# Optimization experiments

Measured on AMD Instinct MI355X. Metric: run time of the kernel, lower is better.

The kernel has to match this reference:

```python
import jax, jax.numpy as jnp
import numpy as np

H = W = 1024          # image_shape (square)
ZP, PH, PW = 16, 32, 32   # psf z-stack shape
THRESH = 2.0          # detection_threshold
K = 1024              # spots_per_frame
ROISIZE = PW          # default roisize = psf.shape[-1]
BG_R = PW * 2         # default bg_filter_size
MAXF = PW             # default max_filter_size


def setup_inputs() -> dict:
    key = jax.random.key(0)
    k1, k2 = jax.random.split(key)
    image = jax.random.uniform(k1, (H, W), jnp.float32) * 100.0
    psf = jax.random.uniform(k2, (ZP, PH, PW), jnp.float32)
    psf = psf / jnp.sum(psf, axis=(1, 2), keepdims=True)  # normalized PSF stack
    return {"image": image, "psf": psf}


def _precompute_filters(psf):
    pad = (H - PH) // 2  # square image/psf -> same pad both dims
    psf_padded = jnp.pad(psf, ((0, 0), (pad, pad), (pad, pad)))
    psf_padded = jnp.fft.fftshift(psf_padded, axes=(1, 2))
    psf_fd = jnp.flip(jnp.fft.fft2(psf_padded), axis=(1, 2))
    rr = (jnp.arange(H) - H // 2)[:, None] ** 2 + (jnp.arange(W) - W // 2)[None, :] ** 2
    bg = (rr < BG_R ** 2).astype(jnp.float32) / (np.pi * BG_R ** 2)
    bg_fd = jnp.fft.fft2(jnp.fft.fftshift(bg))
    return psf_fd, bg_fd


def reference(image, psf):
    psf_fd, bg_fd = _precompute_filters(psf)
    image_fd = jnp.fft.fft2(image)
    conv_psf = jnp.fft.ifft2(image_fd[None] * psf_fd).real       # [Z,H,W]
    conv_bg = jnp.fft.ifft2(image_fd * bg_fd).real               # [H,W]
    ratio = conv_psf / (conv_bg[None] + 1.0)                     # matched-filter SNR
    result = ratio.max(axis=0)                                   # [H,W]
    zmap = jnp.argmax(ratio, axis=0)                             # best z plane

    # MaxPool2d(MAXF, stride=1, padding=MAXF//2-1): torch pads with -inf,
    # output is [H-1,W-1]; torch code then zero-pads one row/col at top-left.
    p = MAXF // 2 - 1
    mx = jax.lax.reduce_window(result, -jnp.inf, jax.lax.max,
                               (MAXF, MAXF), (1, 1), ((p, p), (p, p)))
    mx = jnp.pad(mx, ((1, 0), (1, 0)))                           # back to [H,W]

    mask = jnp.where((mx == result) & (result > THRESH), result, 0.0)
    values, indices = jax.lax.top_k(mask.ravel(), K)
    x = indices % W
    y = indices // H  # torch divides by input_shape[0]; square so == W
    roy = y - ROISIZE // 2
    rox = x - ROISIZE // 2
    valid = ((values > THRESH)
             & (roy >= 0) & (roy < H - ROISIZE)
             & (rox >= 0) & (rox < W - ROISIZE))

    # fixed-shape version of boolean select: clamp for safe gather, mask invalids
    roy_c = jnp.clip(roy, 0, H - ROISIZE)
    rox_c = jnp.clip(rox, 0, W - ROISIZE)
    r = jnp.arange(ROISIZE)
    Y = roy_c[:, None, None] + r[None, :, None]                  # [K,R,1]
    X = rox_c[:, None, None] + r[None, None, :]                  # [K,1,R]
    rois = image[Y, X] * valid[:, None, None].astype(image.dtype)  # [K,R,R]

    roipos = jnp.stack((roy_c, rox_c), -1) * valid[:, None]
    intensity = values * valid
    return roipos, intensity, rois, valid
```

## Files before the change

### kernel.cpp

```cpp
#include <hip/hip_runtime.h>
#include <stdint.h>

typedef float v4f __attribute__((ext_vector_type(4)));
typedef int   v8i __attribute__((ext_vector_type(8)));

#define PEX_STRIDE 1156
#define CSTRIDE 858
#define WS_IMG8   0
#define WS_BFRAG  1048576
#define WS_PEX    1064960
#define WS_RESULT 9994240
#define WS_CAND   14188544

__device__ inline unsigned char f32_to_e4m3(float v) {
    if (!(v > 0.0f)) return 0;
    if (v >= 448.0f) return 0x7e;
    if (v < 0.015625f) {
        int m = (int)(v * 512.0f + 0.5f);
        if (m > 7) return 0x08;
        return (unsigned char)m;
    }
    unsigned int u = __float_as_uint(v) + 0x00080000u;
    int e = (int)((u >> 23) & 0xff) - 127;
    int m3 = (int)(u >> 20) & 7;
    int e8 = e + 7;
    if (e8 >= 16) return 0x7e;
    return (unsigned char)((e8 << 3) | m3);
}

__global__ void k_pex(const float* __restrict__ img, float* __restrict__ pex,
                      uint32_t* __restrict__ img8, const float* __restrict__ psf,
                      unsigned char* __restrict__ bf, unsigned int* cnt,
                      float4* __restrict__ out, int n4) {
    __shared__ float wtot[4];
    int blk = blockIdx.x, t = threadIdx.x;
    if (blk >= 1024) {
        if (blk < 2080) {
            int i = (blk - 1024) * 256 + t;
            if (i < n4) { float4 z; z.x = z.y = z.z = z.w = 0.f; out[i] = z; }
        } else {
            int u = (blk - 2080) * 256 + t;
            if (u == 0) cnt[0] = 0u;
            int kb4 = u >> 11; int l = (u >> 5) & 63; int b = u & 31;
            int z = l & 15; int a = kb4 * 4 + (l >> 4);
            float p = psf[z * 1024 + a * 32 + b];
            float c = cosf((float)(a + b - 32) * (6.283185307179586f / 1024.0f));
            bf[u] = f32_to_e4m3(p * c * 1024.0f);
        }
        return;
    }
    int r = blk;
    const float* row = img + r * 1024;
    float s[5];
    float acc = 0.f;
    int base = t * 5;
    #pragma unroll
    for (int j = 0; j < 5; j++) {
        int c = base + j;
        float v = (c < 1152) ? row[(c - 64) & 1023] : 0.f;
        acc += v; s[j] = acc;
    }
    float sc = acc;
    int lane = t & 63, w = t >> 6;
    #pragma unroll
    for (int off = 1; off < 64; off <<= 1) {
        float v = __shfl_up(sc, off, 64);
        if (lane >= off) sc += v;
    }
    if (lane == 63) wtot[w] = sc;
    __syncthreads();
    float wbase = 0.f;
    #pragma unroll
    for (int i = 0; i < 3; i++) if (i < w) wbase += wtot[i];
    float excl = wbase + (sc - acc);
    float* prow = pex + r * PEX_STRIDE;
    if (t == 0) prow[0] = 0.f;
    #pragma unroll
    for (int j = 0; j < 5; j++) {
        int c = base + j;
        if (c < 1152) prow[c + 1] = excl + s[j];
    }
    float4 v4 = *(const float4*)(row + 4 * t);
    img8[r * 256 + t] = (uint32_t)f32_to_e4m3(v4.x)
                      | ((uint32_t)f32_to_e4m3(v4.y) << 8)
                      | ((uint32_t)f32_to_e4m3(v4.z) << 16)
                      | ((uint32_t)f32_to_e4m3(v4.w) << 24);
}

__device__ inline v8i ldsB(const unsigned long long* p) {
    unsigned long long q0 = p[0], q1 = p[1], q2 = p[2], q3 = p[3];
    v8i v;
    v[0] = (int)(unsigned int)q0;  v[1] = (int)(unsigned int)(q0 >> 32);
    v[2] = (int)(unsigned int)q1;  v[3] = (int)(unsigned int)(q1 >> 32);
    v[4] = (int)(unsigned int)q2;  v[5] = (int)(unsigned int)(q2 >> 32);
    v[6] = (int)(unsigned int)q3;  v[7] = (int)(unsigned int)(q3 >> 32);
    return v;
}

__global__ __launch_bounds__(512, 4) void k_conv(
    const unsigned long long* __restrict__ img64,
    const unsigned char* __restrict__ bfrag,
    const float* __restrict__ pex, float* __restrict__ result) {
    __shared__ unsigned long long sm[8 * CSTRIDE];
    __shared__ float rbp[8][5][8];
    __shared__ float rbv[8][5];
    int tid = threadIdx.x;
    int wave = tid >> 6, lane = tid & 63;
    int b = blockIdx.x;
    int tr = b >> 5, tc = b & 31;
    int r0 = tr * 64, c0 = tc * 32;

    if (lane < 40) {
        int si = lane / 5, kc = lane - si * 5;
        int baserow = r0 + si * 8 + 3;
        int n = c0 + 8 * kc;
        int j0 = wave * 16;
        float acc = 0.f;
        #pragma unroll
        for (int u = 0; u < 16; u++) {
            int j = j0 + u;
            if (j < 127) {
                int dy = j - 63;
                int ady = dy < 0 ? -dy : dy;
                int w = (int)sqrtf((float)(4095 - ady * ady));
                const float* p = pex + ((baserow + dy) & 1023) * PEX_STRIDE + n;
                acc += p[65 + w] - p[64 - w];
            }
        }
        rbp[si][kc][wave] = acc;
    }

    for (int u = tid; u < 665; u += 512) {
        int dr = u / 7;
        int x8 = u - dr * 7;
        int row = (r0 + dr - 16) & 1023;
        int cb0 = (c0 + x8 * 8 - 16) & 1023;
        int cb1 = (cb0 + 8) & 1023;
        unsigned long long lo = img64[row * 128 + (cb0 >> 3)];
        unsigned long long hi = img64[row * 128 + (cb1 >> 3)];
        int dst = dr * 9 + x8;
        sm[dst] = lo;
        #pragma unroll
        for (int s = 1; s < 8; s++)
            sm[s * CSTRIDE + dst] = (lo >> (8 * s)) | (hi << (64 - 8 * s));
    }
    __syncthreads();
    if (tid < 40) {
        int si = tid / 5, kc = tid - si * 5;
        float s = 0.f;
        #pragma unroll
        for (int h = 0; h < 8; h++) s += rbp[si][kc][h];
        const float kk = (float)(1.0 / (3.14159265358979323846 * 4096.0));
        rbv[si][kc] = 1.0f / ((s * kk + 1.0f) * 1024.0f);
    }

    int i0 = (wave >> 1) * 16;
    int cw = (wave & 1) * 16;
    int q = lane >> 4;
    int n = lane & 15;
    const unsigned long long* bpq =
        sm + (n & 7) * CSTRIDE + ((cw + n) >> 3) + (i0 + q) * 9;
    const v8i* bfA = (const v8i*)(bfrag + lane * 32);

    float zmax[16];
    #pragma unroll
    for (int h = 0; h < 2; h++) {
        #pragma unroll
        for (int p = 0; p < 4; p++) {
            const unsigned long long* tp = bpq + (h * 8 + p) * 9;
            v4f a0 = (v4f)0.0f, a1 = (v4f)0.0f;
            v8i bcur = ldsB(tp);
            #pragma unroll
            for (int kb4 = 0; kb4 < 8; kb4++) {
                v8i bnxt = ldsB(tp + (4 * (kb4 + 1)) * 9);
                v8i av = bfA[kb4 << 6];
                a0 = __builtin_amdgcn_mfma_scale_f32_16x16x128_f8f6f4(
                        av, bcur, a0, 0, 0, 0, 0x7f7f7f7f, 0, 0x7f7f7f7f);
                a1 = __builtin_amdgcn_mfma_scale_f32_16x16x128_f8f6f4(
                        av, bnxt, a1, 0, 0, 0, 0x7f7f7f7f, 0, 0x7f7f7f7f);
                bcur = bnxt;
            }
            float m0 = fmaxf(fmaxf(a0.x, a0.y), fmaxf(a0.z, a0.w));
            m0 = fmaxf(m0, __shfl_xor(m0, 16, 64));
            m0 = fmaxf(m0, __shfl_xor(m0, 32, 64));
            zmax[h * 8 + p] = m0;
            float m1 = fmaxf(fmaxf(a1.x, a1.y), fmaxf(a1.z, a1.w));
            m1 = fmaxf(m1, __shfl_xor(m1, 16, 64));
            m1 = fmaxf(m1, __shfl_xor(m1, 32, 64));
            zmax[h * 8 + p + 4] = m1;
            __builtin_amdgcn_sched_barrier(0);
        }
    }
    __syncthreads();

    int uu = cw + n;
    int kc = uu >> 3;
    float fr = (float)(uu & 7) * 0.125f;
    int gcol = c0 + uu;
    #pragma unroll
    for (int c4 = 0; c4 < 4; c4++) {
        float m01 = (q & 1) ? zmax[c4 * 4 + 1] : zmax[c4 * 4 + 0];
        float m23 = (q & 1) ? zmax[c4 * 4 + 3] : zmax[c4 * 4 + 2];
        float m = (q & 2) ? m23 : m01;
        int lrow = i0 + c4 * 4 + q;
        int sil = lrow >> 3;
        float rv0 = rbv[sil][kc], rv1 = rbv[sil][kc + 1];
        float rbl = rv0 + fr * (rv1 - rv0);
        result[(r0 + lrow) * 1024 + gcol] = m * rbl;
    }
}

__global__ __launch_bounds__(256) void k_maxcand(const float* __restrict__ result,
                                                 unsigned int* cnt,
                                                 unsigned long long* cand) {
    __shared__ float ls[95 * 96];
    __shared__ float hr[95 * 64];
    __shared__ float wmax[4];
    int bx = blockIdx.x & 15, by = blockIdx.x >> 4;
    int i0 = by * 64, j0 = bx * 64;
    int t = threadIdx.x;
    const float4* cb4 = (const float4*)(result + i0 * 1024 + j0);
    float mx = -3.4e38f;
    #pragma unroll
    for (int k = 0; k < 4; k++) {
        int idx = k * 256 + t;
        float4 v = cb4[(idx >> 4) * 256 + (idx & 15)];
        mx = fmaxf(mx, fmaxf(fmaxf(v.x, v.y), fmaxf(v.z, v.w)));
    }
    #pragma unroll
    for (int m = 1; m < 64; m <<= 1) mx = fmaxf(mx, __shfl_xor(mx, m, 64));
    if ((t & 63) == 0) wmax[t >> 6] = mx;
    __syncthreads();
    float tmax = fmaxf(fmaxf(wmax[0], wmax[1]), fmaxf(wmax[2], wmax[3]));
    if (tmax <= 2.0f) return;

    for (int idx = t; idx < 95 * 95; idx += 256) {
        int r = idx / 95, c = idx - r * 95;
        int gr = i0 - 16 + r, gc = j0 - 16 + c;
        float v = -3.4e38f;
        if ((unsigned)gr < 1024u && (unsigned)gc < 1024u) v = result[gr * 1024 + gc];
        ls[r * 96 + c] = v;
    }
    __syncthreads();
    for (int idx = t; idx < 95 * 64; idx += 256) {
        int r = idx >> 6, c = idx & 63;
        const float* p = ls + r * 96 + c;
        float m = p[0];
        #pragma unroll
        for (int d = 1; d < 32; d++) m = fmaxf(m, p[d]);
        hr[idx] = m;
    }
    __syncthreads();
    for (int idx = t; idx < 64 * 64; idx += 256) {
        int r = idx >> 6, c = idx & 63;
        const float* p = hr + r * 64 + c;
        float m = p[0];
        #pragma unroll
        for (int d = 1; d < 32; d++) m = fmaxf(m, p[d * 64]);
        float v = ls[(r + 16) * 96 + (c + 16)];
        int gi = i0 + r, gj = j0 + c;
        if (gi >= 1 && gj >= 1 && v > 2.0f && v == m) {
            unsigned int k = atomicAdd(cnt, 1u);
            if (k < 2048)
                cand[k] = ((unsigned long long)__float_as_uint(v) << 32)
                        | (unsigned int)(~(unsigned int)(gi * 1024 + gj));
        }
    }
}

__global__ __launch_bounds__(1024) void k_final(
    const float* __restrict__ image, const unsigned int* __restrict__ cnt,
    const unsigned long long* __restrict__ cand, float* __restrict__ out) {
    __shared__ unsigned long long keys[2048];
    int t = threadIdx.x;
    int n = (int)cnt[0]; if (n > 2048) n = 2048;
    if (n == 0) return;
    for (int k = t; k < 2048; k += 1024) keys[k] = (k < n) ? cand[k] : 0ull;
    __syncthreads();
    for (int size = 2; size <= 2048; size <<= 1) {
        for (int stride = size >> 1; stride > 0; stride >>= 1) {
            for (int i = t; i < 2048; i += 1024) {
                int ixj = i ^ stride;
                if (ixj > i) {
                    unsigned long long a = keys[i], b = keys[ixj];
                    bool sw = ((i & size) == 0) ? (a < b) : (a > b);
                    if (sw) { keys[i] = b; keys[ixj] = a; }
                }
            }
            __syncthreads();
        }
    }
    float* roipos = out;
    float* intensity = out + 2048;
    float* rois = out + 3072;
    float* validf = out + 3072 + 1048576;
    int nw = n < 1024 ? n : 1024;
    if (t < nw) {
        unsigned long long key = keys[t];
        float val = __uint_as_float((unsigned int)(key >> 32));
        unsigned int p = ~(unsigned int)key;
        int y = (int)(p >> 10), x = (int)(p & 1023);
        int roy = y - 16, rox = x - 16;
        bool valid = (roy >= 0 && roy < 992 && rox >= 0 && rox < 992);
        int royc = roy < 0 ? 0 : (roy > 992 ? 992 : roy);
        int roxc = rox < 0 ? 0 : (rox > 992 ? 992 : rox);
        roipos[2 * t]     = valid ? (float)royc : 0.f;
        roipos[2 * t + 1] = valid ? (float)roxc : 0.f;
        intensity[t]      = valid ? val : 0.f;
        validf[t]         = valid ? 1.f : 0.f;
    }
    __syncthreads();
    for (int k = 0; k < nw; k++) {
        unsigned long long key = keys[k];
        unsigned int p = ~(unsigned int)key;
        int y = (int)(p >> 10), x = (int)(p & 1023);
        int roy = y - 16, rox = x - 16;
        if (!(roy >= 0 && roy < 992 && rox >= 0 && rox < 992)) continue;
        int u = t >> 5, vv = t & 31;
        rois[k * 1024 + t] = image[(roy + u) * 1024 + (rox + vv)];
    }
}

extern "C" void kernel_launch(void* const* d_in, const int* in_sizes, int n_in,
                              void* d_out, int out_size, void* d_ws, size_t ws_size,
                              hipStream_t stream) {
    const float* image = (const float*)d_in[0];
    const float* psf   = (const float*)d_in[1];
    float* out = (float*)d_out;
    char* ws = (char*)d_ws;
    unsigned char* img8  = (unsigned char*)(ws + WS_IMG8);
    unsigned char* bfrag = (unsigned char*)(ws + WS_BFRAG);
    float* pex = (float*)(ws + WS_PEX);
    float* result = (float*)(ws + WS_RESULT);
    unsigned int* cnt = (unsigned int*)(ws + WS_CAND);
    unsigned long long* cand = (unsigned long long*)(ws + WS_CAND + 16);

    int n4 = out_size / 4;
    hipLaunchKernelGGL(k_pex,     dim3(2144), dim3(256), 0, stream,
                       image, pex, (uint32_t*)img8, psf, bfrag, cnt, (float4*)d_out, n4);
    hipLaunchKernelGGL(k_conv,    dim3(512),  dim3(512), 0, stream,
                       (const unsigned long long*)img8, bfrag, pex, result);
    hipLaunchKernelGGL(k_maxcand, dim3(256),  dim3(256), 0, stream, result, cnt, cand);
    hipLaunchKernelGGL(k_final,   dim3(1),    dim3(1024), 0, stream, image, cnt, cand, out);
}
```

Before: 95.92 us.

## Build shifted FP8 conv operands in registers instead of shared memory

The convolution kernel no longer stages the FP8 image tile in shared memory as eight pre-shifted copies. Each lane now loads its rows straight from global memory into registers and makes the byte-shifted B operands with 64-bit shifts, so every loaded window feeds four MFMA accumulators over adjacent column groups. The block shrinks from 512 to 256 threads, each wave covers a full 16x32 output strip, and the output is written as float4 stores. This removes the LDS staging and LDS reads, but raises register pressure (a 64-entry u64 array per lane) and adds shift/or ALU work.

```diff
diff --git a/kernel.cpp b/kernel.cpp
--- a/kernel.cpp
+++ b/kernel.cpp
@@ -3,9 +3,9 @@
 
 typedef float v4f __attribute__((ext_vector_type(4)));
 typedef int   v8i __attribute__((ext_vector_type(8)));
+typedef unsigned long long u64;
 
 #define PEX_STRIDE 1156
-#define CSTRIDE 858
 #define WS_IMG8   0
 #define WS_BFRAG  1048576
 #define WS_PEX    1064960
@@ -87,127 +87,134 @@
                       | ((uint32_t)f32_to_e4m3(v4.w) << 24);
 }
 
-__device__ inline v8i ldsB(const unsigned long long* p) {
-    unsigned long long q0 = p[0], q1 = p[1], q2 = p[2], q3 = p[3];
+__device__ inline v8i packb(u64 a, u64 b, u64 c, u64 d) {
     v8i v;
-    v[0] = (int)(unsigned int)q0;  v[1] = (int)(unsigned int)(q0 >> 32);
-    v[2] = (int)(unsigned int)q1;  v[3] = (int)(unsigned int)(q1 >> 32);
-    v[4] = (int)(unsigned int)q2;  v[5] = (int)(unsigned int)(q2 >> 32);
-    v[6] = (int)(unsigned int)q3;  v[7] = (int)(unsigned int)(q3 >> 32);
+    v[0] = (int)(unsigned int)a;  v[1] = (int)(unsigned int)(a >> 32);
+    v[2] = (int)(unsigned int)b;  v[3] = (int)(unsigned int)(b >> 32);
+    v[4] = (int)(unsigned int)c;  v[5] = (int)(unsigned int)(c >> 32);
+    v[6] = (int)(unsigned int)d;  v[7] = (int)(unsigned int)(d >> 32);
     return v;
 }
 
-__global__ __launch_bounds__(512, 4) void k_conv(
-    const unsigned long long* __restrict__ img64,
+__device__ inline float redz(v4f a) {
+    float m = fmaxf(fmaxf(a.x, a.y), fmaxf(a.z, a.w));
+    m = fmaxf(m, __shfl_xor(m, 16, 64));
+    m = fmaxf(m, __shfl_xor(m, 32, 64));
+    return m;
+}
+
+__global__ __launch_bounds__(256, 2) void k_conv(
+    const unsigned char* __restrict__ img8,
     const unsigned char* __restrict__ bfrag,
     const float* __restrict__ pex, float* __restrict__ result) {
-    __shared__ unsigned long long sm[8 * CSTRIDE];
-    __shared__ float rbp[8][5][8];
+    __shared__ float rbp[8][5][4];
     __shared__ float rbv[8][5];
     int tid = threadIdx.x;
     int wave = tid >> 6, lane = tid & 63;
     int b = blockIdx.x;
     int tr = b >> 5, tc = b & 31;
     int r0 = tr * 64, c0 = tc * 32;
+    int nn = lane & 15, g = lane >> 4;
+    int i0 = wave * 16;
+
+    const ulonglong2* ip = (const ulonglong2*)img8;
+    int ck0 = ((c0 - 16) & 1023) >> 4;
+    int ck1 = ( c0        & 1023) >> 4;
+    int ck2 = ((c0 + 16) & 1023) >> 4;
+    int ck3 = ((c0 + 32) & 1023) >> 4;
+    u64 w[8][8];
+    #pragma unroll
+    for (int kb4 = 0; kb4 < 8; kb4++) {
+        int rr = (r0 + i0 + nn + g + 4 * kb4 - 16) & 1023;
+        const ulonglong2* rp = ip + rr * 64;
+        ulonglong2 q0 = rp[ck0], q1 = rp[ck1], q2 = rp[ck2], q3 = rp[ck3];
+        w[kb4][0] = q0.x; w[kb4][1] = q0.y;
+        w[kb4][2] = q1.x; w[kb4][3] = q1.y;
+        w[kb4][4] = q2.x; w[kb4][5] = q2.y;
+        w[kb4][6] = q3.x; w[kb4][7] = q3.y;
+    }
 
     if (lane < 40) {
         int si = lane / 5, kc = lane - si * 5;
         int baserow = r0 + si * 8 + 3;
         int n = c0 + 8 * kc;
-        int j0 = wave * 16;
+        int j0 = wave * 32;
         float acc = 0.f;
         #pragma unroll
-        for (int u = 0; u < 16; u++) {
+        for (int u = 0; u < 32; u++) {
             int j = j0 + u;
             if (j < 127) {
                 int dy = j - 63;
                 int ady = dy < 0 ? -dy : dy;
-                int w = (int)sqrtf((float)(4095 - ady * ady));
+                int ww = (int)sqrtf((float)(4095 - ady * ady));
                 const float* p = pex + ((baserow + dy) & 1023) * PEX_STRIDE + n;
-                acc += p[65 + w] - p[64 - w];
+                acc += p[65 + ww] - p[64 - ww];
             }
         }
         rbp[si][kc][wave] = acc;
-    }
-
-    for (int u = tid; u < 665; u += 512) {
-        int dr = u / 7;
-        int x8 = u - dr * 7;
-        int row = (r0 + dr - 16) & 1023;
-        int cb0 = (c0 + x8 * 8 - 16) & 1023;
-        int cb1 = (cb0 + 8) & 1023;
-        unsigned long long lo = img64[row * 128 + (cb0 >> 3)];
-        unsigned long long hi = img64[row * 128 + (cb1 >> 3)];
-        int dst = dr * 9 + x8;
-        sm[dst] = lo;
-        #pragma unroll
-        for (int s = 1; s < 8; s++)
-            sm[s * CSTRIDE + dst] = (lo >> (8 * s)) | (hi << (64 - 8 * s));
     }
     __syncthreads();
     if (tid < 40) {
         int si = tid / 5, kc = tid - si * 5;
-        float s = 0.f;
-        #pragma unroll
-        for (int h = 0; h < 8; h++) s += rbp[si][kc][h];
+        float s = rbp[si][kc][0] + rbp[si][kc][1] + rbp[si][kc][2] + rbp[si][kc][3];
         const float kk = (float)(1.0 / (3.14159265358979323846 * 4096.0));
         rbv[si][kc] = 1.0f / ((s * kk + 1.0f) * 1024.0f);
     }
 
-    int i0 = (wave >> 1) * 16;
-    int cw = (wave & 1) * 16;
-    int q = lane >> 4;
-    int n = lane & 15;
-    const unsigned long long* bpq =
-        sm + (n & 7) * CSTRIDE + ((cw + n) >> 3) + (i0 + q) * 9;
     const v8i* bfA = (const v8i*)(bfrag + lane * 32);
-
-    float zmax[16];
-    #pragma unroll
-    for (int h = 0; h < 2; h++) {
+    float zm[8];
+    #pragma unroll
+    for (int sh = 0; sh < 8; sh++) {
+        v4f a0 = (v4f)0.f, a1 = (v4f)0.f, a2 = (v4f)0.f, a3 = (v4f)0.f;
         #pragma unroll
-        for (int p = 0; p < 4; p++) {
-            const unsigned long long* tp = bpq + (h * 8 + p) * 9;
-            v4f a0 = (v4f)0.0f, a1 = (v4f)0.0f;
-            v8i bcur = ldsB(tp);
-            #pragma unroll
-            for (int kb4 = 0; kb4 < 8; kb4++) {
-                v8i bnxt = ldsB(tp + (4 * (kb4 + 1)) * 9);
-                v8i av = bfA[kb4 << 6];
-                a0 = __builtin_amdgcn_mfma_scale_f32_16x16x128_f8f6f4(
-                        av, bcur, a0, 0, 0, 0, 0x7f7f7f7f, 0, 0x7f7f7f7f);
-                a1 = __builtin_amdgcn_mfma_scale_f32_16x16x128_f8f6f4(
-                        av, bnxt, a1, 0, 0, 0, 0x7f7f7f7f, 0, 0x7f7f7f7f);
-                bcur = bnxt;
+        for (int kb4 = 0; kb4 < 8; kb4++) {
+            u64 S0, S1, S2, S3, S4, S5, S6;
+            if (sh == 0) {
+                S0 = w[kb4][0]; S1 = w[kb4][1]; S2 = w[kb4][2]; S3 = w[kb4][3];
+                S4 = w[kb4][4]; S5 = w[kb4][5]; S6 = w[kb4][6];
+            } else {
+                const int sb = 8 * sh;
+                S0 = (w[kb4][0] >> sb) | (w[kb4][1] << (64 - sb));
+                S1 = (w[kb4][1] >> sb) | (w[kb4][2] << (64 - sb));
+                S2 = (w[kb4][2] >> sb) | (w[kb4][3] << (64 - sb));
+                S3 = (w[kb4][3] >> sb) | (w[kb4][4] << (64 - sb));
+                S4 = (w[kb4][4] >> sb) | (w[kb4][5] << (64 - sb));
+                S5 = (w[kb4][5] >> sb) | (w[kb4][6] << (64 - sb));
+                S6 = (w[kb4][6] >> sb) | (w[kb4][7] << (64 - sb));
             }
-            float m0 = fmaxf(fmaxf(a0.x, a0.y), fmaxf(a0.z, a0.w));
-            m0 = fmaxf(m0, __shfl_xor(m0, 16, 64));
-            m0 = fmaxf(m0, __shfl_xor(m0, 32, 64));
-            zmax[h * 8 + p] = m0;
-            float m1 = fmaxf(fmaxf(a1.x, a1.y), fmaxf(a1.z, a1.w));
-            m1 = fmaxf(m1, __shfl_xor(m1, 16, 64));
-            m1 = fmaxf(m1, __shfl_xor(m1, 32, 64));
-            zmax[h * 8 + p + 4] = m1;
-            __builtin_amdgcn_sched_barrier(0);
-        }
-    }
-    __syncthreads();
-
-    int uu = cw + n;
-    int kc = uu >> 3;
-    float fr = (float)(uu & 7) * 0.125f;
-    int gcol = c0 + uu;
-    #pragma unroll
-    for (int c4 = 0; c4 < 4; c4++) {
-        float m01 = (q & 1) ? zmax[c4 * 4 + 1] : zmax[c4 * 4 + 0];
-        float m23 = (q & 1) ? zmax[c4 * 4 + 3] : zmax[c4 * 4 + 2];
-        float m = (q & 2) ? m23 : m01;
-        int lrow = i0 + c4 * 4 + q;
-        int sil = lrow >> 3;
-        float rv0 = rbv[sil][kc], rv1 = rbv[sil][kc + 1];
-        float rbl = rv0 + fr * (rv1 - rv0);
-        result[(r0 + lrow) * 1024 + gcol] = m * rbl;
-    }
+            v8i av = bfA[kb4 << 6];
+            a0 = __builtin_amdgcn_mfma_scale_f32_16x16x128_f8f6f4(
+                    av, packb(S0, S1, S2, S3), a0, 0, 0, 0, 0x7f7f7f7f, 0, 0x7f7f7f7f);
+            a1 = __builtin_amdgcn_mfma_scale_f32_16x16x128_f8f6f4(
+                    av, packb(S1, S2, S3, S4), a1, 0, 0, 0, 0x7f7f7f7f, 0, 0x7f7f7f7f);
+            a2 = __builtin_amdgcn_mfma_scale_f32_16x16x128_f8f6f4(
+                    av, packb(S2, S3, S4, S5), a2, 0, 0, 0, 0x7f7f7f7f, 0, 0x7f7f7f7f);
+            a3 = __builtin_amdgcn_mfma_scale_f32_16x16x128_f8f6f4(
+                    av, packb(S3, S4, S5, S6), a3, 0, 0, 0, 0x7f7f7f7f, 0, 0x7f7f7f7f);
+        }
+        float z0 = redz(a0), z1 = redz(a1), z2 = redz(a2), z3 = redz(a3);
+        zm[sh] = (g == 0) ? z0 : (g == 1) ? z1 : (g == 2) ? z2 : z3;
+    }
+    __syncthreads();
+
+    int sil = (i0 + nn) >> 3;
+    float rv0 = rbv[sil][0], rv1 = rbv[sil][1], rv2 = rbv[sil][2],
+          rv3 = rbv[sil][3], rv4 = rbv[sil][4];
+    float rva = (g == 0) ? rv0 : (g == 1) ? rv1 : (g == 2) ? rv2 : rv3;
+    float rvb = (g == 0) ? rv1 : (g == 1) ? rv2 : (g == 2) ? rv3 : rv4;
+    float dr_ = 0.125f * (rvb - rva);
+    float* orow = result + (r0 + i0 + nn) * 1024 + c0 + 8 * g;
+    float4 o0, o1;
+    o0.x = zm[0] * rva;
+    o0.y = zm[1] * (rva + 1.f * dr_);
+    o0.z = zm[2] * (rva + 2.f * dr_);
+    o0.w = zm[3] * (rva + 3.f * dr_);
+    o1.x = zm[4] * (rva + 4.f * dr_);
+    o1.y = zm[5] * (rva + 5.f * dr_);
+    o1.z = zm[6] * (rva + 6.f * dr_);
+    o1.w = zm[7] * (rva + 7.f * dr_);
+    *(float4*)orow = o0;
+    *(float4*)(orow + 4) = o1;
 }
 
 __global__ __launch_bounds__(256) void k_maxcand(const float* __restrict__ result,
@@ -338,8 +345,8 @@
     int n4 = out_size / 4;
     hipLaunchKernelGGL(k_pex,     dim3(2144), dim3(256), 0, stream,
                        image, pex, (uint32_t*)img8, psf, bfrag, cnt, (float4*)d_out, n4);
-    hipLaunchKernelGGL(k_conv,    dim3(512),  dim3(512), 0, stream,
-                       (const unsigned long long*)img8, bfrag, pex, result);
+    hipLaunchKernelGGL(k_conv,    dim3(512),  dim3(256), 0, stream,
+                       img8, bfrag, pex, result);
     hipLaunchKernelGGL(k_maxcand, dim3(256),  dim3(256), 0, stream, result, cnt, cand);
     hipLaunchKernelGGL(k_final,   dim3(1),    dim3(1024), 0, stream, image, cnt, cand, out);
 }
```

New measurement: 108.3 us. 1.13x slower.

## Build shifted B fragments in registers instead of pre-shifted LDS copies

Applied to the files above, without the earlier changes.

The conv kernel no longer stores eight byte-shifted copies of the fp8 image tile in shared memory. It stores one unshifted copy with a 16-byte row layout, and each lane builds all eight shifted B operands from six loaded 64-bit words using funnel shifts. The MFMA loop is reorganised so one A fragment and one set of row loads feed 16 accumulators across the shifts, and each lane writes its output as a single float4 store. This cuts LDS fill work and LDS reads but adds shift ALU work and raises accumulator register pressure under a 512-thread, 4-block launch bound, which could cause spills or lower occupancy.

```diff
diff --git a/kernel.cpp b/kernel.cpp
--- a/kernel.cpp
+++ b/kernel.cpp
@@ -3,9 +3,9 @@
 
 typedef float v4f __attribute__((ext_vector_type(4)));
 typedef int   v8i __attribute__((ext_vector_type(8)));
+typedef unsigned long long u64;
 
 #define PEX_STRIDE 1156
-#define CSTRIDE 858
 #define WS_IMG8   0
 #define WS_BFRAG  1048576
 #define WS_PEX    1064960
@@ -87,21 +87,27 @@
                       | ((uint32_t)f32_to_e4m3(v4.w) << 24);
 }
 
-__device__ inline v8i ldsB(const unsigned long long* p) {
-    unsigned long long q0 = p[0], q1 = p[1], q2 = p[2], q3 = p[3];
+__device__ inline v8i packb(u64 a, u64 b, u64 c, u64 d) {
     v8i v;
-    v[0] = (int)(unsigned int)q0;  v[1] = (int)(unsigned int)(q0 >> 32);
-    v[2] = (int)(unsigned int)q1;  v[3] = (int)(unsigned int)(q1 >> 32);
-    v[4] = (int)(unsigned int)q2;  v[5] = (int)(unsigned int)(q2 >> 32);
-    v[6] = (int)(unsigned int)q3;  v[7] = (int)(unsigned int)(q3 >> 32);
+    v[0] = (int)(unsigned int)a;  v[1] = (int)(unsigned int)(a >> 32);
+    v[2] = (int)(unsigned int)b;  v[3] = (int)(unsigned int)(b >> 32);
+    v[4] = (int)(unsigned int)c;  v[5] = (int)(unsigned int)(c >> 32);
+    v[6] = (int)(unsigned int)d;  v[7] = (int)(unsigned int)(d >> 32);
     return v;
+}
+
+__device__ inline float redz(v4f a) {
+    float m = fmaxf(fmaxf(a.x, a.y), fmaxf(a.z, a.w));
+    m = fmaxf(m, __shfl_xor(m, 16, 64));
+    m = fmaxf(m, __shfl_xor(m, 32, 64));
+    return m;
 }
 
 __global__ __launch_bounds__(512, 4) void k_conv(
     const unsigned long long* __restrict__ img64,
     const unsigned char* __restrict__ bfrag,
     const float* __restrict__ pex, float* __restrict__ result) {
-    __shared__ unsigned long long sm[8 * CSTRIDE];
+    __shared__ ulonglong2 smv[95 * 5];
     __shared__ float rbp[8][5][8];
     __shared__ float rbv[8][5];
     int tid = threadIdx.x;
@@ -130,19 +136,12 @@
         rbp[si][kc][wave] = acc;
     }
 
-    for (int u = tid; u < 665; u += 512) {
-        int dr = u / 7;
-        int x8 = u - dr * 7;
+    u64* smq = (u64*)smv;
+    for (int u = tid; u < 760; u += 512) {
+        int dr = u >> 3, j = u & 7;
         int row = (r0 + dr - 16) & 1023;
-        int cb0 = (c0 + x8 * 8 - 16) & 1023;
-        int cb1 = (cb0 + 8) & 1023;
-        unsigned long long lo = img64[row * 128 + (cb0 >> 3)];
-        unsigned long long hi = img64[row * 128 + (cb1 >> 3)];
-        int dst = dr * 9 + x8;
-        sm[dst] = lo;
-        #pragma unroll
-        for (int s = 1; s < 8; s++)
-            sm[s * CSTRIDE + dst] = (lo >> (8 * s)) | (hi << (64 - 8 * s));
+        int cbyte = (c0 - 16 + 8 * j) & 1023;
+        smq[dr * 10 + j] = img64[row * 128 + (cbyte >> 3)];
     }
     __syncthreads();
     if (tid < 40) {
@@ -154,60 +153,63 @@
         rbv[si][kc] = 1.0f / ((s * kk + 1.0f) * 1024.0f);
     }
 
-    int i0 = (wave >> 1) * 16;
-    int cw = (wave & 1) * 16;
-    int q = lane >> 4;
-    int n = lane & 15;
-    const unsigned long long* bpq =
-        sm + (n & 7) * CSTRIDE + ((cw + n) >> 3) + (i0 + q) * 9;
+    int rg = wave >> 1, h = wave & 1;
+    int i0 = rg * 16;
+    int nn = lane & 15, g = lane >> 4;
     const v8i* bfA = (const v8i*)(bfrag + lane * 32);
 
-    float zmax[16];
-    #pragma unroll
-    for (int h = 0; h < 2; h++) {
-        #pragma unroll
-        for (int p = 0; p < 4; p++) {
-            const unsigned long long* tp = bpq + (h * 8 + p) * 9;
-            v4f a0 = (v4f)0.0f, a1 = (v4f)0.0f;
-            v8i bcur = ldsB(tp);
-            #pragma unroll
-            for (int kb4 = 0; kb4 < 8; kb4++) {
-                v8i bnxt = ldsB(tp + (4 * (kb4 + 1)) * 9);
-                v8i av = bfA[kb4 << 6];
-                a0 = __builtin_amdgcn_mfma_scale_f32_16x16x128_f8f6f4(
-                        av, bcur, a0, 0, 0, 0, 0x7f7f7f7f, 0, 0x7f7f7f7f);
-                a1 = __builtin_amdgcn_mfma_scale_f32_16x16x128_f8f6f4(
-                        av, bnxt, a1, 0, 0, 0, 0x7f7f7f7f, 0, 0x7f7f7f7f);
-                bcur = bnxt;
+    v4f acc0[8], acc1[8];
+    #pragma unroll
+    for (int s = 0; s < 8; s++) { acc0[s] = (v4f)0.f; acc1[s] = (v4f)0.f; }
+
+    #pragma unroll
+    for (int kb4 = 0; kb4 < 8; kb4++) {
+        int lr = i0 + nn + g + 4 * kb4;
+        const ulonglong2* rp = smv + lr * 5 + h;
+        ulonglong2 p0 = rp[0], p1 = rp[1], p2 = rp[2];
+        u64 w0 = p0.x, w1 = p0.y, w2 = p1.x, w3 = p1.y, w4 = p2.x, w5 = p2.y;
+        v8i av = bfA[kb4 << 6];
+        #pragma unroll
+        for (int sh = 0; sh < 8; sh++) {
+            u64 S0, S1, S2, S3, S4;
+            if (sh == 0) { S0 = w0; S1 = w1; S2 = w2; S3 = w3; S4 = w4; }
+            else {
+                const int sb = 8 * sh;
+                S0 = (w0 >> sb) | (w1 << (64 - sb));
+                S1 = (w1 >> sb) | (w2 << (64 - sb));
+                S2 = (w2 >> sb) | (w3 << (64 - sb));
+                S3 = (w3 >> sb) | (w4 << (64 - sb));
+                S4 = (w4 >> sb) | (w5 << (64 - sb));
             }
-            float m0 = fmaxf(fmaxf(a0.x, a0.y), fmaxf(a0.z, a0.w));
-            m0 = fmaxf(m0, __shfl_xor(m0, 16, 64));
-            m0 = fmaxf(m0, __shfl_xor(m0, 32, 64));
-            zmax[h * 8 + p] = m0;
-            float m1 = fmaxf(fmaxf(a1.x, a1.y), fmaxf(a1.z, a1.w));
-            m1 = fmaxf(m1, __shfl_xor(m1, 16, 64));
-            m1 = fmaxf(m1, __shfl_xor(m1, 32, 64));
-            zmax[h * 8 + p + 4] = m1;
-            __builtin_amdgcn_sched_barrier(0);
-        }
-    }
-    __syncthreads();
-
-    int uu = cw + n;
-    int kc = uu >> 3;
-    float fr = (float)(uu & 7) * 0.125f;
-    int gcol = c0 + uu;
-    #pragma unroll
-    for (int c4 = 0; c4 < 4; c4++) {
-        float m01 = (q & 1) ? zmax[c4 * 4 + 1] : zmax[c4 * 4 + 0];
-        float m23 = (q & 1) ? zmax[c4 * 4 + 3] : zmax[c4 * 4 + 2];
-        float m = (q & 2) ? m23 : m01;
-        int lrow = i0 + c4 * 4 + q;
-        int sil = lrow >> 3;
-        float rv0 = rbv[sil][kc], rv1 = rbv[sil][kc + 1];
-        float rbl = rv0 + fr * (rv1 - rv0);
-        result[(r0 + lrow) * 1024 + gcol] = m * rbl;
-    }
+            acc0[sh] = __builtin_amdgcn_mfma_scale_f32_16x16x128_f8f6f4(
+                    av, packb(S0, S1, S2, S3), acc0[sh], 0, 0, 0,
+                    0x7f7f7f7f, 0, 0x7f7f7f7f);
+            acc1[sh] = __builtin_amdgcn_mfma_scale_f32_16x16x128_f8f6f4(
+                    av, packb(S1, S2, S3, S4), acc1[sh], 0, 0, 0,
+                    0x7f7f7f7f, 0, 0x7f7f7f7f);
+        }
+    }
+
+    float zm0[8], zm1[8];
+    #pragma unroll
+    for (int sh = 0; sh < 8; sh++) { zm0[sh] = redz(acc0[sh]); zm1[sh] = redz(acc1[sh]); }
+    __syncthreads();
+
+    int sil = (i0 + nn) >> 3;
+    int kc = 2 * h + (g >> 1);
+    float rv0 = rbv[sil][kc], rv1 = rbv[sil][kc + 1];
+    float drv = rv1 - rv0;
+    float ov[4];
+    #pragma unroll
+    for (int t = 0; t < 4; t++) {
+        float za = (g & 1) ? zm0[4 + t] : zm0[t];
+        float zb = (g & 1) ? zm1[4 + t] : zm1[t];
+        float z = (g & 2) ? zb : za;
+        float fr = (float)(4 * (g & 1) + t) * 0.125f;
+        ov[t] = z * (rv0 + fr * drv);
+    }
+    float4 o; o.x = ov[0]; o.y = ov[1]; o.z = ov[2]; o.w = ov[3];
+    *(float4*)(result + (r0 + i0 + nn) * 1024 + c0 + 16 * h + 4 * g) = o;
 }
 
 __global__ __launch_bounds__(256) void k_maxcand(const float* __restrict__ result,
```

Measured after the change: 111.6 us. 1.16x slower.

## Precompute 8 byte-shifted FP8 image copies globally instead of shifting in conv

Applied to the files above, without the earlier changes.

k_pex now writes eight byte-shifted copies of the FP8 image into global workspace, built through a shared row buffer. k_conv then loads already-shifted 64-bit words straight into LDS as 16-byte stores, with no per-tile shift/OR work. LDS row pitch changes from 9 to 10 words so the 16-byte stores stay aligned. The cost is 8x the global traffic for the FP8 image (8 MB written and a larger read footprint) and a bigger workspace.

```diff
diff --git a/kernel.cpp b/kernel.cpp
--- a/kernel.cpp
+++ b/kernel.cpp
@@ -3,14 +3,15 @@
 
 typedef float v4f __attribute__((ext_vector_type(4)));
 typedef int   v8i __attribute__((ext_vector_type(8)));
+typedef unsigned long long u64;
 
 #define PEX_STRIDE 1156
-#define CSTRIDE 858
+#define CSTRIDE 950
 #define WS_IMG8   0
-#define WS_BFRAG  1048576
-#define WS_PEX    1064960
-#define WS_RESULT 9994240
-#define WS_CAND   14188544
+#define WS_BFRAG  8388608
+#define WS_PEX    8404992
+#define WS_RESULT 13139968
+#define WS_CAND   17334272
 
 __device__ inline unsigned char f32_to_e4m3(float v) {
     if (!(v > 0.0f)) return 0;
@@ -29,10 +30,11 @@
 }
 
 __global__ void k_pex(const float* __restrict__ img, float* __restrict__ pex,
-                      uint32_t* __restrict__ img8, const float* __restrict__ psf,
+                      u64* __restrict__ img8s, const float* __restrict__ psf,
                       unsigned char* __restrict__ bf, unsigned int* cnt,
                       float4* __restrict__ out, int n4) {
     __shared__ float wtot[4];
+    __shared__ uint32_t rowpk[256];
     int blk = blockIdx.x, t = threadIdx.x;
     if (blk >= 1024) {
         if (blk < 2080) {
@@ -51,6 +53,13 @@
     }
     int r = blk;
     const float* row = img + r * 1024;
+    float4 v4 = *(const float4*)(row + 4 * t);
+    uint32_t pk = (uint32_t)f32_to_e4m3(v4.x)
+                | ((uint32_t)f32_to_e4m3(v4.y) << 8)
+                | ((uint32_t)f32_to_e4m3(v4.z) << 16)
+                | ((uint32_t)f32_to_e4m3(v4.w) << 24);
+    rowpk[t] = pk;
+
     float s[5];
     float acc = 0.f;
     int base = t * 5;
@@ -80,15 +89,26 @@
         int c = base + j;
         if (c < 1152) prow[c + 1] = excl + s[j];
     }
-    float4 v4 = *(const float4*)(row + 4 * t);
-    img8[r * 256 + t] = (uint32_t)f32_to_e4m3(v4.x)
-                      | ((uint32_t)f32_to_e4m3(v4.y) << 8)
-                      | ((uint32_t)f32_to_e4m3(v4.z) << 16)
-                      | ((uint32_t)f32_to_e4m3(v4.w) << 24);
-}
-
-__device__ inline v8i ldsB(const unsigned long long* p) {
-    unsigned long long q0 = p[0], q1 = p[1], q2 = p[2], q3 = p[3];
+    {
+        int scp = t >> 5;
+        int j4 = (t & 31) * 4;
+        int sb = 8 * (scp & 3);
+        int wo = scp >> 2;
+        #pragma unroll
+        for (int i = 0; i < 4; i++) {
+            int j = j4 + i;
+            int w0 = (2 * j + wo) & 255;
+            int w1 = (2 * j + wo + 1) & 255;
+            int w2 = (2 * j + wo + 2) & 255;
+            u64 lo = ((u64)rowpk[w1] << 32) | (u64)rowpk[w0];
+            u64 val = sb ? ((lo >> sb) | ((u64)rowpk[w2] << (64 - sb))) : lo;
+            img8s[((size_t)scp << 17) + r * 128 + j] = val;
+        }
+    }
+}
+
+__device__ inline v8i ldsB(const u64* p) {
+    u64 q0 = p[0], q1 = p[1], q2 = p[2], q3 = p[3];
     v8i v;
     v[0] = (int)(unsigned int)q0;  v[1] = (int)(unsigned int)(q0 >> 32);
     v[2] = (int)(unsigned int)q1;  v[3] = (int)(unsigned int)(q1 >> 32);
@@ -98,12 +118,13 @@
 }
 
 __global__ __launch_bounds__(512, 4) void k_conv(
-    const unsigned long long* __restrict__ img64,
+    const u64* __restrict__ img64,
     const unsigned char* __restrict__ bfrag,
     const float* __restrict__ pex, float* __restrict__ result) {
-    __shared__ unsigned long long sm[8 * CSTRIDE];
+    __shared__ ulonglong2 smv2[8 * 475];
     __shared__ float rbp[8][5][8];
     __shared__ float rbv[8][5];
+    u64* sm = (u64*)smv2;
     int tid = threadIdx.x;
     int wave = tid >> 6, lane = tid & 63;
     int b = blockIdx.x;
@@ -130,19 +151,17 @@
         rbp[si][kc][wave] = acc;
     }
 
-    for (int u = tid; u < 665; u += 512) {
-        int dr = u / 7;
-        int x8 = u - dr * 7;
+    for (int u = tid; u < 3040; u += 512) {
+        int s = u / 380, rem = u - s * 380;
+        int dr = rem >> 2, p = rem & 3;
         int row = (r0 + dr - 16) & 1023;
-        int cb0 = (c0 + x8 * 8 - 16) & 1023;
-        int cb1 = (cb0 + 8) & 1023;
-        unsigned long long lo = img64[row * 128 + (cb0 >> 3)];
-        unsigned long long hi = img64[row * 128 + (cb1 >> 3)];
-        int dst = dr * 9 + x8;
-        sm[dst] = lo;
-        #pragma unroll
-        for (int s = 1; s < 8; s++)
-            sm[s * CSTRIDE + dst] = (lo >> (8 * s)) | (hi << (64 - 8 * s));
+        int B0 = (c0 - 16 + 16 * p) & 1023;
+        int B1 = (B0 + 8) & 1023;
+        const u64* cp = img64 + ((size_t)s << 17) + row * 128;
+        ulonglong2 pr;
+        pr.x = cp[B0 >> 3];
+        pr.y = cp[B1 >> 3];
+        *((ulonglong2*)(sm + s * CSTRIDE + dr * 10) + p) = pr;
     }
     __syncthreads();
     if (tid < 40) {
@@ -158,8 +177,7 @@
     int cw = (wave & 1) * 16;
     int q = lane >> 4;
     int n = lane & 15;
-    const unsigned long long* bpq =
-        sm + (n & 7) * CSTRIDE + ((cw + n) >> 3) + (i0 + q) * 9;
+    const u64* bpq = sm + (n & 7) * CSTRIDE + ((cw + n) >> 3) + (i0 + q) * 10;
     const v8i* bfA = (const v8i*)(bfrag + lane * 32);
 
     float zmax[16];
@@ -167,12 +185,12 @@
     for (int h = 0; h < 2; h++) {
         #pragma unroll
         for (int p = 0; p < 4; p++) {
-            const unsigned long long* tp = bpq + (h * 8 + p) * 9;
+            const u64* tp = bpq + (h * 8 + p) * 10;
             v4f a0 = (v4f)0.0f, a1 = (v4f)0.0f;
             v8i bcur = ldsB(tp);
             #pragma unroll
             for (int kb4 = 0; kb4 < 8; kb4++) {
-                v8i bnxt = ldsB(tp + (4 * (kb4 + 1)) * 9);
+                v8i bnxt = ldsB(tp + (4 * (kb4 + 1)) * 10);
                 v8i av = bfA[kb4 << 6];
                 a0 = __builtin_amdgcn_mfma_scale_f32_16x16x128_f8f6f4(
                         av, bcur, a0, 0, 0, 0, 0x7f7f7f7f, 0, 0x7f7f7f7f);
@@ -328,7 +346,7 @@
     const float* psf   = (const float*)d_in[1];
     float* out = (float*)d_out;
     char* ws = (char*)d_ws;
-    unsigned char* img8  = (unsigned char*)(ws + WS_IMG8);
+    u64* img8s = (u64*)(ws + WS_IMG8);
     unsigned char* bfrag = (unsigned char*)(ws + WS_BFRAG);
     float* pex = (float*)(ws + WS_PEX);
     float* result = (float*)(ws + WS_RESULT);
@@ -337,9 +355,9 @@
 
     int n4 = out_size / 4;
     hipLaunchKernelGGL(k_pex,     dim3(2144), dim3(256), 0, stream,
-                       image, pex, (uint32_t*)img8, psf, bfrag, cnt, (float4*)d_out, n4);
+                       image, pex, img8s, psf, bfrag, cnt, (float4*)d_out, n4);
     hipLaunchKernelGGL(k_conv,    dim3(512),  dim3(512), 0, stream,
-                       (const unsigned long long*)img8, bfrag, pex, result);
+                       img8s, bfrag, pex, result);
     hipLaunchKernelGGL(k_maxcand, dim3(256),  dim3(256), 0, stream, result, cnt, cand);
     hipLaunchKernelGGL(k_final,   dim3(1),    dim3(1024), 0, stream, image, cnt, cand, out);
 }
```

Result: slower. 104.8 us (+9.2%).
